# Kernel tuning notes

Hardware: AMD Instinct MI355X
Metric: run time of the kernel (lower is better)

Reference implementation:

```python
import jax, jax.numpy as jnp
import numpy as np
import math

B, N, D, H = 4, 2048, 256, 4
DH = D // H
EPS = 1e-8


def setup_inputs() -> dict:
    key = jax.random.key(0)
    ks = jax.random.split(key, 8)
    x = jax.random.normal(ks[0], (B, N, D), dtype=jnp.float32)
    # RoPE rotation freqs: exp(i * pos * inv_freq), stored as (cos, sin) pairs -> [N, DH//2, 2]
    d2 = DH // 2
    inv_freq = 1.0 / (10000.0 ** (jnp.arange(d2, dtype=jnp.float32) / d2))
    ang = jnp.arange(N, dtype=jnp.float32)[:, None] * inv_freq[None, :]
    freqs = jnp.stack([jnp.cos(ang), jnp.sin(ang)], axis=-1)  # [N, d2, 2]
    s = 0.02
    g = jnp.ones((D,), dtype=jnp.float32)
    w_qkv = jax.random.normal(ks[1], (D, 3 * D), dtype=jnp.float32) * s
    b_qkv = jnp.zeros((3 * D,), dtype=jnp.float32)
    w_out = jax.random.normal(ks[2], (D, D), dtype=jnp.float32) * s
    b_out = jnp.zeros((D,), dtype=jnp.float32)
    w_gate = jax.random.normal(ks[3], (D, D), dtype=jnp.float32) * s
    b_gate = jnp.zeros((D,), dtype=jnp.float32)
    return {"x": x, "freqs": freqs, "g": g, "w_qkv": w_qkv, "b_qkv": b_qkv,
            "w_out": w_out, "b_out": b_out, "w_gate": w_gate, "b_gate": b_gate}


def _zcrmsnorm(x, g):
    x0 = x - jnp.mean(x, axis=-1, keepdims=True)
    rms = jnp.sqrt(jnp.mean(x0 * x0, axis=-1, keepdims=True) + EPS)
    return x0 / rms * g


def _rope(q, freqs):
    # q: [B,H,N,DH]; freqs: [N,DH//2,2] (cos,sin). Complex multiply on adjacent pairs.
    b, h, n, dh = q.shape
    qp = q.reshape(b, h, n, dh // 2, 2)
    cos = freqs[:n, :, 0][None, None]  # [1,1,N,d2]
    sin = freqs[:n, :, 1][None, None]
    q0, q1 = qp[..., 0], qp[..., 1]
    out = jnp.stack([q0 * cos - q1 * sin, q0 * sin + q1 * cos], axis=-1)
    return out.reshape(b, h, n, dh)


def reference(x, freqs, g, w_qkv, b_qkv, w_out, b_out, w_gate, b_gate):
    b, n, d = x.shape
    h = _zcrmsnorm(x, g)
    qkv = (h @ w_qkv + b_qkv).reshape(b, n, 3, H, DH)
    qkv = jnp.transpose(qkv, (2, 0, 3, 1, 4))  # [3,B,H,N,DH]
    q, k, v = qkv[0], qkv[1], qkv[2]
    q = _rope(q, freqs)
    k = _rope(k, freqs)
    scores = jnp.einsum('bhqd,bhkd->bhqk', q, k) / math.sqrt(DH)
    attn = jax.nn.softmax(scores, axis=-1)  # dropout is identity in eval
    y = jnp.einsum('bhqk,bhkd->bhqd', attn, v)
    y = jnp.transpose(y, (0, 2, 1, 3)).reshape(b, n, d)
    y = y @ w_out + b_out
    gate = jax.nn.sigmoid(h @ w_gate + b_gate)
    return x + gate * y
```

## Files before the change

### kernel.cpp

```cpp
#include <hip/hip_runtime.h>

typedef unsigned short u16;
typedef unsigned int u32;
typedef short short8 __attribute__((ext_vector_type(8)));
typedef float f32x4 __attribute__((ext_vector_type(4)));
typedef float f32x16 __attribute__((ext_vector_type(16)));

#define B_ 4
#define N_ 2048
#define D_ 256
#define H_ 4
#define DH_ 64
#define BN_ 8192

__device__ inline float b2f(u16 u) {
    union { u32 i; float f; } v; v.i = ((u32)u) << 16; return v.f;
}
__device__ inline u16 f2b(float f) {
    union { float f; u32 i; } v; v.f = f;
    return (u16)((v.i + 0x8000u) >> 16);
}
__device__ inline u32 pkbf(float a, float b) {
    union { float f; u32 i; } ua, ub; ua.f = a; ub.f = b;
    return __builtin_amdgcn_perm(ub.i + 0x8000u, ua.i + 0x8000u, 0x07060302u);
}
__device__ inline f32x4 mfma16(short8 a, short8 b, f32x4 c) {
    return __builtin_amdgcn_mfma_f32_16x16x32_bf16(a, b, c, 0, 0, 0);
}
__device__ inline f32x16 mfma32(short8 a, short8 b, f32x16 c) {
    return __builtin_amdgcn_mfma_f32_32x32x16_bf16(a, b, c, 0, 0, 0);
}

#define QSCALE 0.18033688f

__global__ __launch_bounds__(256) void gemm_front(
    const u16* __restrict__ A, const u16* __restrict__ BT,
    const float* __restrict__ b_qkv, const float* __restrict__ b_gate,
    const float* __restrict__ freqs,
    u16* __restrict__ Qb, u16* __restrict__ Kb,
    u16* __restrict__ VT, u16* __restrict__ gatb)
{
    const int tid = threadIdx.x;
    const int wave = tid >> 6, lane = tid & 63;
    const int ln15 = lane & 15, quad = lane >> 4;
    const int by = blockIdx.y;
    const int m0 = blockIdx.x * 128 + (wave & 1) * 64;
    const int n0 = by * 128 + (wave >> 1) * 64;

    const f32x4 zero = {0.f, 0.f, 0.f, 0.f};
    f32x4 acc[4][4];
    #pragma unroll
    for (int i = 0; i < 4; ++i)
        #pragma unroll
        for (int j = 0; j < 4; ++j) acc[i][j] = zero;

    #pragma unroll
    for (int k0 = 0; k0 < 256; k0 += 32) {
        const int koff = k0 + quad * 8;
        short8 a[4], b[4];
        #pragma unroll
        for (int i = 0; i < 4; ++i)
            a[i] = *(const short8*)(A + (size_t)(m0 + i * 16 + ln15) * 256 + koff);
        #pragma unroll
        for (int j = 0; j < 4; ++j)
            b[j] = *(const short8*)(BT + (size_t)(n0 + j * 16 + ln15) * 256 + koff);
        #pragma unroll
        for (int i = 0; i < 4; ++i)
            #pragma unroll
            for (int j = 0; j < 4; ++j)
                acc[i][j] = mfma16(a[i], b[j], acc[i][j]);
    }

    if (by < 4) {
        #pragma unroll
        for (int j = 0; j < 4; ++j) {
            const int c  = n0 + j * 16 + ln15;
            const int hh = (c >> 6) & 3;
            const int dh = c & 63;
            const int d2 = dh >> 1;
            const bool isQ = (c < 256);
            const bool ev  = ((dh & 1) == 0);
            const float bv = b_qkv[c];
            u16* dst = isQ ? Qb : Kb;
            #pragma unroll
            for (int i = 0; i < 4; ++i) {
                const int r = m0 + i * 16 + quad * 4;
                #pragma unroll
                for (int rg = 0; rg < 4; ++rg) {
                    const int t = r + rg;
                    const int n = t & 2047, b = t >> 11;
                    float v = acc[i][j][rg] + bv;
                    float pv = __shfl_xor(v, 1);
                    const float2 cs = *(const float2*)(freqs + (size_t)n * 64 + d2 * 2);
                    float o = ev ? (v * cs.x - pv * cs.y)
                                 : (pv * cs.y + v * cs.x);
                    if (isQ) o *= QSCALE;
                    dst[((size_t)(b * H_ + hh) * N_ + n) * DH_ + dh] = f2b(o);
                }
            }
        }
    } else if (by < 6) {
        #pragma unroll
        for (int j = 0; j < 4; ++j) {
            const int c  = n0 + j * 16 + ln15;
            const int hh = (c >> 6) & 3;
            const int dh = c & 63;
            const float bv = b_qkv[c];
            #pragma unroll
            for (int i = 0; i < 4; ++i) {
                const int r = m0 + i * 16 + quad * 4;
                const int n = r & 2047, b = r >> 11;
                uint2 w;
                w.x = pkbf(acc[i][j][0] + bv, acc[i][j][1] + bv);
                w.y = pkbf(acc[i][j][2] + bv, acc[i][j][3] + bv);
                *(uint2*)(VT + ((size_t)(b * H_ + hh) * DH_ + dh) * N_ + n) = w;
            }
        }
    } else {
        #pragma unroll
        for (int j = 0; j < 4; ++j) {
            const int c  = n0 + j * 16 + ln15;
            const int cg = c - 768;
            const float bv = b_gate[cg];
            #pragma unroll
            for (int i = 0; i < 4; ++i) {
                const int r = m0 + i * 16 + quad * 4;
                #pragma unroll
                for (int rg = 0; rg < 4; ++rg) {
                    float v = acc[i][j][rg] + bv;
                    gatb[(size_t)(r + rg) * 256 + cg] = f2b(1.0f / (1.0f + __expf(-v)));
                }
            }
        }
    }
}

__global__ __launch_bounds__(256) void norm_transw_k(
    const float* __restrict__ x, const float* __restrict__ g, u16* __restrict__ h,
    const float* __restrict__ wqkv, const float* __restrict__ wout,
    const float* __restrict__ wgate,
    u16* __restrict__ wqkvT, u16* __restrict__ woutT, u16* __restrict__ wgateT)
{
    if (blockIdx.x < 2048) {
        const int wave = threadIdx.x >> 6, lane = threadIdx.x & 63;
        const int t = blockIdx.x * 4 + wave;
        const float4 u = *(const float4*)(x + (size_t)t * D_ + lane * 4);
        float s  = u.x + u.y + u.z + u.w;
        float s2 = u.x * u.x + u.y * u.y + u.z * u.z + u.w * u.w;
        #pragma unroll
        for (int m = 1; m < 64; m <<= 1) {
            s  += __shfl_xor(s, m);
            s2 += __shfl_xor(s2, m);
        }
        float mean = s * (1.0f / D_);
        float var  = s2 * (1.0f / D_) - mean * mean;
        float rinv = rsqrtf(var + 1e-8f);
        const float4 gv = *(const float4*)(g + lane * 4);
        uint2 o;
        o.x = pkbf((u.x - mean) * rinv * gv.x, (u.y - mean) * rinv * gv.y);
        o.y = pkbf((u.z - mean) * rinv * gv.z, (u.w - mean) * rinv * gv.w);
        *(uint2*)(h + (size_t)t * D_ + lane * 4) = o;
    } else {
        int idx = (blockIdx.x - 2048) * 256 + threadIdx.x;
        if (idx < 768 * 256) {
            int nn = idx >> 8, kk = idx & 255;
            wqkvT[idx] = f2b(wqkv[kk * 768 + nn]);
        }
        idx -= 768 * 256;
        if (idx >= 0 && idx < 256 * 256) {
            int nn = idx >> 8, kk = idx & 255;
            woutT[idx]  = f2b(wout[kk * 256 + nn]);
            wgateT[idx] = f2b(wgate[kk * 256 + nn]);
        }
    }
}

__global__ __launch_bounds__(256, 4) void attn_k(
    const u16* __restrict__ Q, const u16* __restrict__ K,
    const u16* __restrict__ VT, u16* __restrict__ Opb,
    float* __restrict__ lvp)
{
    __shared__ __align__(16) u16 Ks[2][64][64];
    __shared__ __align__(16) u16 Vs[2][64][64];
    const int tid = threadIdx.x;
    const int wave = tid >> 6, lane = tid & 63;
    const int l31 = lane & 31, hi = lane >> 5;
    const int id = blockIdx.x;
    const int bh   = ((id & 7) << 1) | ((id >> 3) & 1);
    const int quar = (id >> 4) & 3;
    const int q0   = (id >> 6) * 128 + wave * 32;
    const int kt0  = quar * 512;

    const u16* Qh = Q + (size_t)bh * N_ * DH_;
    const u16* Kh = K + (size_t)bh * N_ * DH_;
    const u16* Vh = VT + (size_t)bh * DH_ * N_;

    short8 bq[4];
    #pragma unroll
    for (int kc = 0; kc < 4; ++kc)
        bq[kc] = *(const short8*)(Qh + (size_t)(q0 + l31) * DH_ + kc * 16 + hi * 8);

    f32x16 o0, o1;
    #pragma unroll
    for (int i = 0; i < 16; ++i) { o0[i] = 0.f; o1[i] = 0.f; }
    float lv = 0.f;

    const int srow = tid >> 2, sq4 = tid & 3;
    const int sw = srow & 7;
    const int wg0 = ((sq4) ^ sw) * 8;
    const int wg1 = ((sq4 + 4) ^ sw) * 8;
    const int rsw = l31 & 7;

    {
        uint4 k0 = *(const uint4*)(Kh + (size_t)(kt0 + srow) * DH_ + sq4 * 8);
        uint4 k1 = *(const uint4*)(Kh + (size_t)(kt0 + srow) * DH_ + (sq4 + 4) * 8);
        uint4 v0 = *(const uint4*)(Vh + (size_t)srow * N_ + kt0 + sq4 * 8);
        uint4 v1 = *(const uint4*)(Vh + (size_t)srow * N_ + kt0 + (sq4 + 4) * 8);
        *(uint4*)&Ks[0][srow][wg0] = k0;
        *(uint4*)&Ks[0][srow][wg1] = k1;
        *(uint4*)&Vs[0][srow][wg0] = v0;
        *(uint4*)&Vs[0][srow][wg1] = v1;
    }
    __syncthreads();

    int p = 0;
    for (int c = 0; c < 8; ++c) {
        const bool more = (c + 1 < 8);
        uint4 k0, k1, v0, v1;
        if (more) {
            const int ktn = kt0 + (c + 1) * 64;
            k0 = *(const uint4*)(Kh + (size_t)(ktn + srow) * DH_ + sq4 * 8);
            k1 = *(const uint4*)(Kh + (size_t)(ktn + srow) * DH_ + (sq4 + 4) * 8);
            v0 = *(const uint4*)(Vh + (size_t)srow * N_ + ktn + sq4 * 8);
            v1 = *(const uint4*)(Vh + (size_t)srow * N_ + ktn + (sq4 + 4) * 8);
        }

        #pragma unroll
        for (int g = 0; g < 2; ++g) {
            f32x16 st;
            #pragma unroll
            for (int i = 0; i < 16; ++i) st[i] = 0.f;
            #pragma unroll
            for (int kc = 0; kc < 4; ++kc) {
                const int gran = ((2 * kc + hi) ^ rsw) * 8;
                short8 ka = *(const short8*)&Ks[p][g * 32 + l31][gran];
                st = mfma32(ka, bq[kc], st);
            }
            #pragma unroll
            for (int r = 0; r < 16; ++r) {
                st[r] = exp2f(st[r]);
                lv += st[r];
            }
            #pragma unroll
            for (int kc2 = 0; kc2 < 2; ++kc2) {
                u32 X0, X1, Y0, Y1;
                asm("v_cvt_pk_bf16_f32 %0, %1, %2" : "=v"(X0) : "v"(st[8*kc2+0]), "v"(st[8*kc2+1]));
                asm("v_cvt_pk_bf16_f32 %0, %1, %2" : "=v"(X1) : "v"(st[8*kc2+2]), "v"(st[8*kc2+3]));
                asm("v_cvt_pk_bf16_f32 %0, %1, %2" : "=v"(Y0) : "v"(st[8*kc2+4]), "v"(st[8*kc2+5]));
                asm("v_cvt_pk_bf16_f32 %0, %1, %2" : "=v"(Y1) : "v"(st[8*kc2+6]), "v"(st[8*kc2+7]));
                asm("v_permlane32_swap_b32 %0, %1" : "+v"(X0), "+v"(Y0));
                asm("v_permlane32_swap_b32 %0, %1" : "+v"(X1), "+v"(Y1));
                union { u32 u[4]; short8 s; } bf;
                bf.u[0] = X0; bf.u[1] = X1; bf.u[2] = Y0; bf.u[3] = Y1;
                const int gran = ((2 * (2 * g + kc2) + hi) ^ rsw) * 8;
                short8 va0 = *(const short8*)&Vs[p][l31][gran];
                short8 va1 = *(const short8*)&Vs[p][32 + l31][gran];
                o0 = mfma32(va0, bf.s, o0);
                o1 = mfma32(va1, bf.s, o1);
            }
        }

        if (more) {
            *(uint4*)&Ks[p ^ 1][srow][wg0] = k0;
            *(uint4*)&Ks[p ^ 1][srow][wg1] = k1;
            *(uint4*)&Vs[p ^ 1][srow][wg0] = v0;
            *(uint4*)&Vs[p ^ 1][srow][wg1] = v1;
        }
        __syncthreads();
        p ^= 1;
    }

    lv += __shfl_xor(lv, 32);
    const size_t rowo = ((size_t)(quar * 16 + bh) * N_ + q0 + l31) * DH_;
    #pragma unroll
    for (int go = 0; go < 2; ++go) {
        #pragma unroll
        for (int rq = 0; rq < 4; ++rq) {
            uint2 w;
            if (go == 0) {
                w.x = pkbf(o0[rq*4+0], o0[rq*4+1]);
                w.y = pkbf(o0[rq*4+2], o0[rq*4+3]);
            } else {
                w.x = pkbf(o1[rq*4+0], o1[rq*4+1]);
                w.y = pkbf(o1[rq*4+2], o1[rq*4+3]);
            }
            *(uint2*)(Opb + rowo + go * 32 + 8 * rq + 4 * hi) = w;
        }
    }
    if (hi == 0) lvp[(size_t)(quar * 16 + bh) * N_ + q0 + l31] = lv;
}

__global__ __launch_bounds__(256) void gemm_out(
    const u16* __restrict__ Opb, const float* __restrict__ lvp,
    const u16* __restrict__ BT, const float* __restrict__ bias,
    float* __restrict__ out, const float* __restrict__ xin,
    const u16* __restrict__ gate)
{
    __shared__ __align__(16) u16 As[16][264];
    const int tid = threadIdx.x;
    const int m0 = blockIdx.x * 16;

    {
        const int r  = tid >> 4;
        const int kc = (tid & 15) * 16;
        const int t  = m0 + r;
        const int n  = t & 2047, b = t >> 11;
        const int h  = kc >> 6;
        const int bh = b * 4 + h;
        const int dh = kc & 63;
        float a[16];
        #pragma unroll
        for (int i = 0; i < 16; ++i) a[i] = 0.f;
        float lsum = 0.f;
        #pragma unroll
        for (int pp = 0; pp < 4; ++pp) {
            const size_t base = ((size_t)(pp * 16 + bh) * N_ + n) * DH_ + dh;
            const uint4 u0 = *(const uint4*)(Opb + base);
            const uint4 u1 = *(const uint4*)(Opb + base + 8);
            const u32 uu[8] = {u0.x, u0.y, u0.z, u0.w, u1.x, u1.y, u1.z, u1.w};
            #pragma unroll
            for (int i2 = 0; i2 < 8; ++i2) {
                a[i2 * 2]     += b2f((u16)(uu[i2] & 0xffff));
                a[i2 * 2 + 1] += b2f((u16)(uu[i2] >> 16));
            }
            lsum += lvp[(size_t)(pp * 16 + bh) * N_ + n];
        }
        const float rl = 1.0f / lsum;
        uint4 w0, w1;
        w0.x = pkbf(a[0] * rl,  a[1] * rl);  w0.y = pkbf(a[2] * rl,  a[3] * rl);
        w0.z = pkbf(a[4] * rl,  a[5] * rl);  w0.w = pkbf(a[6] * rl,  a[7] * rl);
        w1.x = pkbf(a[8] * rl,  a[9] * rl);  w1.y = pkbf(a[10] * rl, a[11] * rl);
        w1.z = pkbf(a[12] * rl, a[13] * rl); w1.w = pkbf(a[14] * rl, a[15] * rl);
        *(uint4*)&As[r][kc]     = w0;
        *(uint4*)&As[r][kc + 8] = w1;
    }
    __syncthreads();

    const int wave = tid >> 6, lane = tid & 63;
    const int ln15 = lane & 15, quad = lane >> 4;
    const int n0 = wave * 64;
    const f32x4 zero = {0.f, 0.f, 0.f, 0.f};
    f32x4 acc[4] = {zero, zero, zero, zero};

    #pragma unroll
    for (int k0 = 0; k0 < 256; k0 += 32) {
        const int koff = k0 + quad * 8;
        const short8 a = *(const short8*)&As[ln15][koff];
        #pragma unroll
        for (int j = 0; j < 4; ++j) {
            const short8 bfr = *(const short8*)(BT + (size_t)(n0 + j * 16 + ln15) * 256 + koff);
            acc[j] = mfma16(a, bfr, acc[j]);
        }
    }

    #pragma unroll
    for (int j = 0; j < 4; ++j) {
        const int c = n0 + j * 16 + ln15;
        const float bv = bias[c];
        const int r = quad * 4;
        #pragma unroll
        for (int rg = 0; rg < 4; ++rg) {
            const size_t idx = (size_t)(m0 + r + rg) * 256 + c;
            out[idx] = xin[idx] + b2f(gate[idx]) * (acc[j][rg] + bv);
        }
    }
}

extern "C" void kernel_launch(void* const* d_in, const int* in_sizes, int n_in,
                              void* d_out, int out_size, void* d_ws, size_t ws_size,
                              hipStream_t stream) {
    const float* x      = (const float*)d_in[0];
    const float* freqs  = (const float*)d_in[1];
    const float* g      = (const float*)d_in[2];
    const float* w_qkv  = (const float*)d_in[3];
    const float* b_qkv  = (const float*)d_in[4];
    const float* w_out  = (const float*)d_in[5];
    const float* b_out  = (const float*)d_in[6];
    const float* w_gate = (const float*)d_in[7];
    const float* b_gate = (const float*)d_in[8];
    float* out = (float*)d_out;

    char* ws = (char*)d_ws;
    size_t off = 0;
    auto carve = [&](size_t nelem) -> u16* {
        u16* p = (u16*)(ws + off);
        off += ((nelem * 2 + 255) / 256) * 256;
        return p;
    };
    u16* h      = carve((size_t)BN_ * D_);
    u16* Qb     = carve((size_t)BN_ * D_);
    u16* Kb     = carve((size_t)BN_ * D_);
    u16* VT     = carve((size_t)BN_ * D_);
    u16* gatb   = carve((size_t)BN_ * D_);
    u16* wqkvT  = carve((size_t)768 * 256);
    u16* wgateT = carve((size_t)256 * 256);
    u16* woutT  = carve((size_t)256 * 256);
    u16*   Opb = carve((size_t)4 * 16 * N_ * DH_);
    float* lvp = (float*)carve((size_t)4 * 16 * N_ * 2);

    hipLaunchKernelGGL(norm_transw_k, dim3(3072), dim3(256), 0, stream,
                       x, g, h, w_qkv, w_out, w_gate, wqkvT, woutT, wgateT);
    hipLaunchKernelGGL(gemm_front, dim3(64, 8), dim3(256), 0, stream,
                       h, wqkvT, b_qkv, b_gate, freqs, Qb, Kb, VT, gatb);
    hipLaunchKernelGGL(attn_k, dim3(1024), dim3(256), 0, stream,
                       Qb, Kb, VT, Opb, lvp);
    hipLaunchKernelGGL(gemm_out, dim3(512), dim3(256), 0, stream,
                       Opb, lvp, woutT, b_out, out, x, gatb);
}
```

Baseline: 147.0 us.

## Fuse RMSNorm into front GEMM and split attention keys into eight chunks

Result: slower. 365.6 us (+148.7%).

```diff
diff --git a/kernel.cpp b/kernel.cpp
--- a/kernel.cpp
+++ b/kernel.cpp
@@ -33,19 +33,66 @@
 
 #define QSCALE 0.18033688f
 
+__global__ __launch_bounds__(256) void transw_k(
+    const float* __restrict__ wqkv, const float* __restrict__ wout,
+    const float* __restrict__ wgate,
+    u16* __restrict__ wqkvT, u16* __restrict__ woutT, u16* __restrict__ wgateT)
+{
+    int idx = blockIdx.x * 256 + threadIdx.x;
+    if (idx < 768 * 256) {
+        int nn = idx >> 8, kk = idx & 255;
+        wqkvT[idx] = f2b(wqkv[kk * 768 + nn]);
+    }
+    idx -= 768 * 256;
+    if (idx >= 0 && idx < 256 * 256) {
+        int nn = idx >> 8, kk = idx & 255;
+        woutT[idx]  = f2b(wout[kk * 256 + nn]);
+        wgateT[idx] = f2b(wgate[kk * 256 + nn]);
+    }
+}
+
 __global__ __launch_bounds__(256) void gemm_front(
-    const u16* __restrict__ A, const u16* __restrict__ BT,
+    const float* __restrict__ x, const float* __restrict__ gw,
+    const u16* __restrict__ BT,
     const float* __restrict__ b_qkv, const float* __restrict__ b_gate,
     const float* __restrict__ freqs,
     u16* __restrict__ Qb, u16* __restrict__ Kb,
     u16* __restrict__ VT, u16* __restrict__ gatb)
 {
+    __shared__ __align__(16) u16 As[128][264];
     const int tid = threadIdx.x;
     const int wave = tid >> 6, lane = tid & 63;
     const int ln15 = lane & 15, quad = lane >> 4;
     const int by = blockIdx.y;
-    const int m0 = blockIdx.x * 128 + (wave & 1) * 64;
-    const int n0 = by * 128 + (wave >> 1) * 64;
+    const int mb = blockIdx.x * 128;
+
+    {
+        const float4 gv = *(const float4*)(gw + lane * 4);
+        #pragma unroll 4
+        for (int rr = 0; rr < 32; ++rr) {
+            const int r = wave * 32 + rr;
+            const float4 u = *(const float4*)(x + (size_t)(mb + r) * D_ + lane * 4);
+            float s  = u.x + u.y + u.z + u.w;
+            float s2 = u.x * u.x + u.y * u.y + u.z * u.z + u.w * u.w;
+            #pragma unroll
+            for (int m = 1; m < 64; m <<= 1) {
+                s  += __shfl_xor(s, m);
+                s2 += __shfl_xor(s2, m);
+            }
+            const float mean = s * (1.0f / D_);
+            const float var  = s2 * (1.0f / D_) - mean * mean;
+            const float rinv = rsqrtf(var + 1e-8f);
+            uint2 o;
+            o.x = pkbf((u.x - mean) * rinv * gv.x, (u.y - mean) * rinv * gv.y);
+            o.y = pkbf((u.z - mean) * rinv * gv.z, (u.w - mean) * rinv * gv.w);
+            *(uint2*)&As[r][lane * 4] = o;
+        }
+    }
+    __syncthreads();
+
+    const int ml0 = (wave & 1) * 64;
+    const int m0  = mb + ml0;
+    const int n0  = by * 128 + (wave >> 1) * 64;
 
     const f32x4 zero = {0.f, 0.f, 0.f, 0.f};
     f32x4 acc[4][4];
@@ -60,7 +107,7 @@
         short8 a[4], b[4];
         #pragma unroll
         for (int i = 0; i < 4; ++i)
-            a[i] = *(const short8*)(A + (size_t)(m0 + i * 16 + ln15) * 256 + koff);
+            a[i] = *(const short8*)&As[ml0 + i * 16 + ln15][koff];
         #pragma unroll
         for (int j = 0; j < 4; ++j)
             b[j] = *(const short8*)(BT + (size_t)(n0 + j * 16 + ln15) * 256 + koff);
@@ -135,61 +182,21 @@
     }
 }
 
-__global__ __launch_bounds__(256) void norm_transw_k(
-    const float* __restrict__ x, const float* __restrict__ g, u16* __restrict__ h,
-    const float* __restrict__ wqkv, const float* __restrict__ wout,
-    const float* __restrict__ wgate,
-    u16* __restrict__ wqkvT, u16* __restrict__ woutT, u16* __restrict__ wgateT)
-{
-    if (blockIdx.x < 2048) {
-        const int wave = threadIdx.x >> 6, lane = threadIdx.x & 63;
-        const int t = blockIdx.x * 4 + wave;
-        const float4 u = *(const float4*)(x + (size_t)t * D_ + lane * 4);
-        float s  = u.x + u.y + u.z + u.w;
-        float s2 = u.x * u.x + u.y * u.y + u.z * u.z + u.w * u.w;
-        #pragma unroll
-        for (int m = 1; m < 64; m <<= 1) {
-            s  += __shfl_xor(s, m);
-            s2 += __shfl_xor(s2, m);
-        }
-        float mean = s * (1.0f / D_);
-        float var  = s2 * (1.0f / D_) - mean * mean;
-        float rinv = rsqrtf(var + 1e-8f);
-        const float4 gv = *(const float4*)(g + lane * 4);
-        uint2 o;
-        o.x = pkbf((u.x - mean) * rinv * gv.x, (u.y - mean) * rinv * gv.y);
-        o.y = pkbf((u.z - mean) * rinv * gv.z, (u.w - mean) * rinv * gv.w);
-        *(uint2*)(h + (size_t)t * D_ + lane * 4) = o;
-    } else {
-        int idx = (blockIdx.x - 2048) * 256 + threadIdx.x;
-        if (idx < 768 * 256) {
-            int nn = idx >> 8, kk = idx & 255;
-            wqkvT[idx] = f2b(wqkv[kk * 768 + nn]);
-        }
-        idx -= 768 * 256;
-        if (idx >= 0 && idx < 256 * 256) {
-            int nn = idx >> 8, kk = idx & 255;
-            woutT[idx]  = f2b(wout[kk * 256 + nn]);
-            wgateT[idx] = f2b(wgate[kk * 256 + nn]);
-        }
-    }
-}
-
-__global__ __launch_bounds__(256, 4) void attn_k(
+__global__ __launch_bounds__(256, 8) void attn_k(
     const u16* __restrict__ Q, const u16* __restrict__ K,
     const u16* __restrict__ VT, u16* __restrict__ Opb,
     float* __restrict__ lvp)
 {
-    __shared__ __align__(16) u16 Ks[2][64][64];
-    __shared__ __align__(16) u16 Vs[2][64][64];
+    __shared__ __align__(16) u16 Ks[2][32][72];
+    __shared__ __align__(16) u16 Vs[2][64][40];
     const int tid = threadIdx.x;
     const int wave = tid >> 6, lane = tid & 63;
     const int l31 = lane & 31, hi = lane >> 5;
     const int id = blockIdx.x;
-    const int bh   = ((id & 7) << 1) | ((id >> 3) & 1);
-    const int quar = (id >> 4) & 3;
-    const int q0   = (id >> 6) * 128 + wave * 32;
-    const int kt0  = quar * 512;
+    const int bh  = ((id & 7) << 1) | ((id >> 3) & 1);
+    const int oct = (id >> 4) & 7;
+    const int q0  = (id >> 7) * 128 + wave * 32;
+    const int kt0 = oct * 256;
 
     const u16* Qh = Q + (size_t)bh * N_ * DH_;
     const u16* Kh = K + (size_t)bh * N_ * DH_;
@@ -205,83 +212,67 @@
     for (int i = 0; i < 16; ++i) { o0[i] = 0.f; o1[i] = 0.f; }
     float lv = 0.f;
 
-    const int srow = tid >> 2, sq4 = tid & 3;
-    const int sw = srow & 7;
-    const int wg0 = ((sq4) ^ sw) * 8;
-    const int wg1 = ((sq4 + 4) ^ sw) * 8;
-    const int rsw = l31 & 7;
+    const int srK = tid >> 3, scK = (tid & 7) * 8;
+    const int srV = tid >> 2, scV = (tid & 3) * 8;
 
     {
-        uint4 k0 = *(const uint4*)(Kh + (size_t)(kt0 + srow) * DH_ + sq4 * 8);
-        uint4 k1 = *(const uint4*)(Kh + (size_t)(kt0 + srow) * DH_ + (sq4 + 4) * 8);
-        uint4 v0 = *(const uint4*)(Vh + (size_t)srow * N_ + kt0 + sq4 * 8);
-        uint4 v1 = *(const uint4*)(Vh + (size_t)srow * N_ + kt0 + (sq4 + 4) * 8);
-        *(uint4*)&Ks[0][srow][wg0] = k0;
-        *(uint4*)&Ks[0][srow][wg1] = k1;
-        *(uint4*)&Vs[0][srow][wg0] = v0;
-        *(uint4*)&Vs[0][srow][wg1] = v1;
+        uint4 kld = *(const uint4*)(Kh + (size_t)(kt0 + srK) * DH_ + scK);
+        uint4 vld = *(const uint4*)(Vh + (size_t)srV * N_ + kt0 + scV);
+        *(uint4*)&Ks[0][srK][scK] = kld;
+        *(uint4*)&Vs[0][srV][scV] = vld;
     }
     __syncthreads();
 
     int p = 0;
     for (int c = 0; c < 8; ++c) {
         const bool more = (c + 1 < 8);
-        uint4 k0, k1, v0, v1;
+        uint4 kld, vld;
         if (more) {
-            const int ktn = kt0 + (c + 1) * 64;
-            k0 = *(const uint4*)(Kh + (size_t)(ktn + srow) * DH_ + sq4 * 8);
-            k1 = *(const uint4*)(Kh + (size_t)(ktn + srow) * DH_ + (sq4 + 4) * 8);
-            v0 = *(const uint4*)(Vh + (size_t)srow * N_ + ktn + sq4 * 8);
-            v1 = *(const uint4*)(Vh + (size_t)srow * N_ + ktn + (sq4 + 4) * 8);
-        }
-
-        #pragma unroll
-        for (int g = 0; g < 2; ++g) {
-            f32x16 st;
-            #pragma unroll
-            for (int i = 0; i < 16; ++i) st[i] = 0.f;
-            #pragma unroll
-            for (int kc = 0; kc < 4; ++kc) {
-                const int gran = ((2 * kc + hi) ^ rsw) * 8;
-                short8 ka = *(const short8*)&Ks[p][g * 32 + l31][gran];
-                st = mfma32(ka, bq[kc], st);
-            }
-            #pragma unroll
-            for (int r = 0; r < 16; ++r) {
-                st[r] = exp2f(st[r]);
-                lv += st[r];
-            }
-            #pragma unroll
-            for (int kc2 = 0; kc2 < 2; ++kc2) {
-                u32 X0, X1, Y0, Y1;
-                asm("v_cvt_pk_bf16_f32 %0, %1, %2" : "=v"(X0) : "v"(st[8*kc2+0]), "v"(st[8*kc2+1]));
-                asm("v_cvt_pk_bf16_f32 %0, %1, %2" : "=v"(X1) : "v"(st[8*kc2+2]), "v"(st[8*kc2+3]));
-                asm("v_cvt_pk_bf16_f32 %0, %1, %2" : "=v"(Y0) : "v"(st[8*kc2+4]), "v"(st[8*kc2+5]));
-                asm("v_cvt_pk_bf16_f32 %0, %1, %2" : "=v"(Y1) : "v"(st[8*kc2+6]), "v"(st[8*kc2+7]));
-                asm("v_permlane32_swap_b32 %0, %1" : "+v"(X0), "+v"(Y0));
-                asm("v_permlane32_swap_b32 %0, %1" : "+v"(X1), "+v"(Y1));
-                union { u32 u[4]; short8 s; } bf;
-                bf.u[0] = X0; bf.u[1] = X1; bf.u[2] = Y0; bf.u[3] = Y1;
-                const int gran = ((2 * (2 * g + kc2) + hi) ^ rsw) * 8;
-                short8 va0 = *(const short8*)&Vs[p][l31][gran];
-                short8 va1 = *(const short8*)&Vs[p][32 + l31][gran];
-                o0 = mfma32(va0, bf.s, o0);
-                o1 = mfma32(va1, bf.s, o1);
-            }
+            const int kb = kt0 + (c + 1) * 32;
+            kld = *(const uint4*)(Kh + (size_t)(kb + srK) * DH_ + scK);
+            vld = *(const uint4*)(Vh + (size_t)srV * N_ + kb + scV);
+        }
+
+        f32x16 st;
+        #pragma unroll
+        for (int i = 0; i < 16; ++i) st[i] = 0.f;
+        #pragma unroll
+        for (int kc = 0; kc < 4; ++kc) {
+            short8 ka = *(const short8*)&Ks[p][l31][kc * 16 + hi * 8];
+            st = mfma32(ka, bq[kc], st);
+        }
+        #pragma unroll
+        for (int r = 0; r < 16; ++r) {
+            st[r] = exp2f(st[r]);
+            lv += st[r];
+        }
+        #pragma unroll
+        for (int kc2 = 0; kc2 < 2; ++kc2) {
+            u32 X0, X1, Y0, Y1;
+            asm("v_cvt_pk_bf16_f32 %0, %1, %2" : "=v"(X0) : "v"(st[8*kc2+0]), "v"(st[8*kc2+1]));
+            asm("v_cvt_pk_bf16_f32 %0, %1, %2" : "=v"(X1) : "v"(st[8*kc2+2]), "v"(st[8*kc2+3]));
+            asm("v_cvt_pk_bf16_f32 %0, %1, %2" : "=v"(Y0) : "v"(st[8*kc2+4]), "v"(st[8*kc2+5]));
+            asm("v_cvt_pk_bf16_f32 %0, %1, %2" : "=v"(Y1) : "v"(st[8*kc2+6]), "v"(st[8*kc2+7]));
+            asm("v_permlane32_swap_b32 %0, %1" : "+v"(X0), "+v"(Y0));
+            asm("v_permlane32_swap_b32 %0, %1" : "+v"(X1), "+v"(Y1));
+            union { u32 u[4]; short8 s; } bf;
+            bf.u[0] = X0; bf.u[1] = X1; bf.u[2] = Y0; bf.u[3] = Y1;
+            short8 va0 = *(const short8*)&Vs[p][l31][(2 * kc2 + hi) * 8];
+            short8 va1 = *(const short8*)&Vs[p][32 + l31][(2 * kc2 + hi) * 8];
+            o0 = mfma32(va0, bf.s, o0);
+            o1 = mfma32(va1, bf.s, o1);
         }
 
         if (more) {
-            *(uint4*)&Ks[p ^ 1][srow][wg0] = k0;
-            *(uint4*)&Ks[p ^ 1][srow][wg1] = k1;
-            *(uint4*)&Vs[p ^ 1][srow][wg0] = v0;
-            *(uint4*)&Vs[p ^ 1][srow][wg1] = v1;
+            *(uint4*)&Ks[p ^ 1][srK][scK] = kld;
+            *(uint4*)&Vs[p ^ 1][srV][scV] = vld;
         }
         __syncthreads();
         p ^= 1;
     }
 
     lv += __shfl_xor(lv, 32);
-    const size_t rowo = ((size_t)(quar * 16 + bh) * N_ + q0 + l31) * DH_;
+    const size_t rowo = ((size_t)(oct * 16 + bh) * N_ + q0 + l31) * DH_;
     #pragma unroll
     for (int go = 0; go < 2; ++go) {
         #pragma unroll
@@ -297,7 +288,7 @@
             *(uint2*)(Opb + rowo + go * 32 + 8 * rq + 4 * hi) = w;
         }
     }
-    if (hi == 0) lvp[(size_t)(quar * 16 + bh) * N_ + q0 + l31] = lv;
+    if (hi == 0) lvp[(size_t)(oct * 16 + bh) * N_ + q0 + l31] = lv;
 }
 
 __global__ __launch_bounds__(256) void gemm_out(
@@ -323,7 +314,7 @@
         for (int i = 0; i < 16; ++i) a[i] = 0.f;
         float lsum = 0.f;
         #pragma unroll
-        for (int pp = 0; pp < 4; ++pp) {
+        for (int pp = 0; pp < 8; ++pp) {
             const size_t base = ((size_t)(pp * 16 + bh) * N_ + n) * DH_ + dh;
             const uint4 u0 = *(const uint4*)(Opb + base);
             const uint4 u1 = *(const uint4*)(Opb + base + 8);
@@ -397,7 +388,6 @@
         off += ((nelem * 2 + 255) / 256) * 256;
         return p;
     };
-    u16* h      = carve((size_t)BN_ * D_);
     u16* Qb     = carve((size_t)BN_ * D_);
     u16* Kb     = carve((size_t)BN_ * D_);
     u16* VT     = carve((size_t)BN_ * D_);
@@ -405,14 +395,14 @@
     u16* wqkvT  = carve((size_t)768 * 256);
     u16* wgateT = carve((size_t)256 * 256);
     u16* woutT  = carve((size_t)256 * 256);
-    u16*   Opb = carve((size_t)4 * 16 * N_ * DH_);
-    float* lvp = (float*)carve((size_t)4 * 16 * N_ * 2);
-
-    hipLaunchKernelGGL(norm_transw_k, dim3(3072), dim3(256), 0, stream,
-                       x, g, h, w_qkv, w_out, w_gate, wqkvT, woutT, wgateT);
+    u16*   Opb = carve((size_t)8 * 16 * N_ * DH_);
+    float* lvp = (float*)carve((size_t)8 * 16 * N_ * 2);
+
+    hipLaunchKernelGGL(transw_k, dim3(1024), dim3(256), 0, stream,
+                       w_qkv, w_out, w_gate, wqkvT, woutT, wgateT);
     hipLaunchKernelGGL(gemm_front, dim3(64, 8), dim3(256), 0, stream,
-                       h, wqkvT, b_qkv, b_gate, freqs, Qb, Kb, VT, gatb);
-    hipLaunchKernelGGL(attn_k, dim3(1024), dim3(256), 0, stream,
+                       x, g, wqkvT, b_qkv, b_gate, freqs, Qb, Kb, VT, gatb);
+    hipLaunchKernelGGL(attn_k, dim3(2048), dim3(256), 0, stream,
                        Qb, Kb, VT, Opb, lvp);
     hipLaunchKernelGGL(gemm_out, dim3(512), dim3(256), 0, stream,
                        Opb, lvp, woutT, b_out, out, x, gatb);
```
